# Optimization experiments

Hardware: AMD Instinct MI355X
Metric: run time of the kernel (lower is better)

## Reference

```python
import jax, jax.numpy as jnp
import numpy as np

E = 1024
B = 16
SV = 576
SL = 448


def setup_inputs() -> dict:
    key = jax.random.key(0)
    k1, k2, k3, k4, k5 = jax.random.split(key, 5)
    return {
        "vision_tokens": jax.random.normal(k1, (B, SV, E), dtype=jnp.float32),
        "language_tokens": jax.random.normal(k2, (B, SL, E), dtype=jnp.float32),
        "Wv": jax.random.normal(k3, (E, E), dtype=jnp.float32) * 0.02,  # vision_proj.weight
        "Wl": jax.random.normal(k4, (E, E), dtype=jnp.float32) * 0.02,  # language_proj.weight
        "Wo": jax.random.normal(k5, (E, E), dtype=jnp.float32) * 0.02,  # out_proj.weight
        "bo": jnp.zeros((E,), dtype=jnp.float32),                        # out_proj.bias
    }


def reference(vision_tokens, language_tokens, Wv, Wl, Wo, bo):
    # Separate modality projections (nn.Linear, no bias): y = x @ W.T
    vp = jnp.einsum("bsd,ed->bse", vision_tokens, Wv)
    lp = jnp.einsum("bsd,ed->bse", language_tokens, Wl)
    # Concat vision+language tokens along sequence dim
    x = jnp.concatenate([vp, lp], axis=1)  # [B, SV+SL, E]
    scale = x.shape[-1] ** -0.5  # 1/sqrt(embed_dim), single-head as in CPU path
    scores = jnp.einsum("bqe,bke->bqk", x, x) * scale
    attn = jax.nn.softmax(scores, axis=-1)
    attended = jnp.einsum("bqk,bke->bqe", attn, x)
    # out_proj (with bias)
    return jnp.einsum("bse,fe->bsf", attended, Wo) + bo
```

## Files before the change

### kernel.cpp

```cpp
#include <hip/hip_runtime.h>

typedef _Float16 f16;
typedef _Float16 f16x4 __attribute__((ext_vector_type(4)));
typedef _Float16 f16x8 __attribute__((ext_vector_type(8)));
typedef float f32x4 __attribute__((ext_vector_type(4)));

#define AS1(p) ((const __attribute__((address_space(1))) void*)(p))
#define AS3(p) ((__attribute__((address_space(3))) void*)(p))
#define BAR() { asm volatile("" ::: "memory"); __builtin_amdgcn_s_barrier(); \
                asm volatile("" ::: "memory"); __builtin_amdgcn_sched_barrier(0); }
#define VMCNT(n) asm volatile("s_waitcnt vmcnt(" #n ")" ::: "memory")


__global__ void conv_f32_to_f16(const float* __restrict__ src, f16* __restrict__ dst, long n4) {
  long i = (long)blockIdx.x * blockDim.x + threadIdx.x;
  if (i >= n4) return;
  const float4 v = ((const float4*)src)[i];
  f16x4 o = { (f16)v.x, (f16)v.y, (f16)v.z, (f16)v.w };
  ((f16x4*)dst)[i] = o;
}

__global__ void conv_tokens(const float* __restrict__ src, f16* __restrict__ dst,
                            int rpb, long dstOff, long n4) {
  long i = (long)blockIdx.x * blockDim.x + threadIdx.x;
  if (i >= n4) return;
  long perB = (long)rpb * 256;
  long b = i / perB, off = i % perB;
  const float4 v = ((const float4*)src)[i];
  f16x4 o = { (f16)v.x, (f16)v.y, (f16)v.z, (f16)v.w };
  ((f16x4*)(dst + b * 1024 * 1024 + dstOff))[off] = o;
}

template<int OUTF>
__global__ __launch_bounds__(512, 2)
void gemm256(const f16* __restrict__ A, const f16* __restrict__ Bw,
             void* __restrict__ Cv, const float* __restrict__ bias,
             int M, long sA, long sB, long sC, float scale)
{
  constexpr int K = 1024, N = 1024, T = K / 64;
  __shared__ __align__(16) char lds[131072];
  const int bz = blockIdx.z;
  const f16* Ab = A + (long)bz * sA;
  const f16* Bb = Bw + (long)bz * sB;
  const int t = threadIdx.x;
  const int w = t >> 6, l = t & 63;
  const int wr = w >> 2, wc = w & 3;
  const int brow = blockIdx.y * 256, bcol = blockIdx.x * 256;

  f32x4 acc[2][4][2][2] = {};

  const int srow = t >> 3;
  const int scol = ((t & 7) * 8) ^ (((t >> 5) & 1) << 4) ^ (((t >> 6) & 1) << 5);
  const int xmask = (((l >> 2) & 1) << 5) | (((l >> 3) & 1) << 6);
  const int lrow = l & 15, lslot = (l >> 4) * 16;

  auto stageA = [&](int kt, int h) {
    char* dst = lds + (kt & 1) * 65536 + h * 16384;
    #pragma unroll
    for (int j = 0; j < 2; ++j) {
      int ar = brow + h * 128 + j * 64 + srow;
      if (ar >= M) ar = M - 1;
      const f16* g = Ab + (long)ar * K + kt * 64 + scol;
      __builtin_amdgcn_global_load_lds(AS1(g), AS3(dst + j * 8192 + t * 16), 16, 0, 0);
    }
  };
  auto stageB = [&](int kt, int h) {
    char* dst = lds + (kt & 1) * 65536 + 32768 + h * 16384;
    #pragma unroll
    for (int j = 0; j < 2; ++j) {
      int br = bcol + h * 128 + j * 64 + srow;
      const f16* g = Bb + (long)br * K + kt * 64 + scol;
      __builtin_amdgcn_global_load_lds(AS1(g), AS3(dst + j * 8192 + t * 16), 16, 0, 0);
    }
  };
  auto ldA = [&](int kt, int mh, f16x8* a) {
    const char* base = lds + (kt & 1) * 65536;
    #pragma unroll
    for (int m4 = 0; m4 < 4; ++m4)
      #pragma unroll
      for (int kk = 0; kk < 2; ++kk) {
        int rowA = mh * 128 + wr * 64 + m4 * 16 + lrow;
        int off = (rowA * 128 + kk * 64 + lslot) ^ xmask;
        a[m4 * 2 + kk] = *(const f16x8*)(base + off);
      }
  };
  auto ldB = [&](int kt, int nh, f16x8* b) {
    const char* base = lds + (kt & 1) * 65536 + 32768;
    #pragma unroll
    for (int n2 = 0; n2 < 2; ++n2)
      #pragma unroll
      for (int kk = 0; kk < 2; ++kk) {
        int rowB = nh * 128 + wc * 32 + n2 * 16 + lrow;
        int off = (rowB * 128 + kk * 64 + lslot) ^ xmask;
        b[n2 * 2 + kk] = *(const f16x8*)(base + off);
      }
  };
  auto mma = [&](int mh, int nh, const f16x8* a, const f16x8* b) {
    __builtin_amdgcn_s_setprio(1);
    #pragma unroll
    for (int m4 = 0; m4 < 4; ++m4)
      #pragma unroll
      for (int n2 = 0; n2 < 2; ++n2)
        #pragma unroll
        for (int kk = 0; kk < 2; ++kk)
          acc[mh][m4][nh][n2] = __builtin_amdgcn_mfma_f32_16x16x32_f16(
              a[m4 * 2 + kk], b[n2 * 2 + kk], acc[mh][m4][nh][n2], 0, 0, 0);
    __builtin_amdgcn_s_setprio(0);
  };

  stageA(0, 0); stageA(0, 1); stageB(0, 0); stageB(0, 1);
  stageA(1, 0); stageB(1, 1);
  VMCNT(4);
  BAR();

  f16x8 a[8], b0[4], b1[4];
  for (int kt = 0; kt < T; ++kt) {
    ldA(kt, 0, a); ldB(kt, 0, b0);
    if (kt + 1 < T) stageA(kt + 1, 1);
    BAR();
    mma(0, 0, a, b0);
    BAR();
    ldB(kt, 1, b1);
    if (kt + 1 < T) stageB(kt + 1, 0);
    BAR();
    mma(0, 1, a, b1);
    BAR();
    ldA(kt, 1, a);
    if (kt + 2 < T) stageA(kt + 2, 0);
    BAR();
    mma(1, 1, a, b1);
    BAR();
    if (kt + 2 < T) {
      stageB(kt + 2, 1);
      VMCNT(4);
    } else if (kt + 1 < T) {
      VMCNT(0);
    }
    BAR();
    mma(1, 0, a, b0);
    BAR();
  }

  const int rj = (l >> 4) * 4;
  #pragma unroll
  for (int mh = 0; mh < 2; ++mh)
    #pragma unroll
    for (int m4 = 0; m4 < 4; ++m4)
      #pragma unroll
      for (int j = 0; j < 4; ++j) {
        const int r = brow + mh * 128 + wr * 64 + m4 * 16 + rj + j;
        if (r >= M) continue;
        #pragma unroll
        for (int nh = 0; nh < 2; ++nh)
          #pragma unroll
          for (int n2 = 0; n2 < 2; ++n2) {
            const int c = bcol + nh * 128 + wc * 32 + n2 * 16 + lrow;
            float v = acc[mh][m4][nh][n2][j];
            if constexpr (OUTF == 0) {
              ((f16*)Cv)[(long)bz * sC + (long)r * N + c] = (f16)v;
            } else if constexpr (OUTF == 1) {
              ((f16*)Cv)[(long)bz * sC + (long)r * N + c] = (f16)(v * scale);
            } else {
              ((float*)Cv)[(long)bz * sC + (long)r * N + c] = v + bias[c];
            }
          }
      }
}

__global__ __launch_bounds__(256)
void softmax_rows(f16* __restrict__ S) {
  const long row = blockIdx.x;
  f16* p = S + row * 1024;
  const int t = threadIdx.x;
  f16x4 v4 = ((f16x4*)p)[t];
  float v[4];
  #pragma unroll
  for (int j = 0; j < 4; ++j) v[j] = (float)v4[j];

  float m = fmaxf(fmaxf(v[0], v[1]), fmaxf(v[2], v[3]));
  #pragma unroll
  for (int off = 1; off < 64; off <<= 1) m = fmaxf(m, __shfl_xor(m, off));
  __shared__ float sm[4], ss[4];
  const int w = t >> 6;
  if ((t & 63) == 0) sm[w] = m;
  __syncthreads();
  m = fmaxf(fmaxf(sm[0], sm[1]), fmaxf(sm[2], sm[3]));

  float e[4], s = 0.f;
  #pragma unroll
  for (int j = 0; j < 4; ++j) { e[j] = __expf(v[j] - m); s += e[j]; }
  #pragma unroll
  for (int off = 1; off < 64; off <<= 1) s += __shfl_xor(s, off);
  if ((t & 63) == 0) ss[w] = s;
  __syncthreads();
  s = ss[0] + ss[1] + ss[2] + ss[3];
  const float inv = 1.f / s;

  f16x4 o;
  #pragma unroll
  for (int j = 0; j < 4; ++j) o[j] = (f16)(e[j] * inv);
  ((f16x4*)p)[t] = o;
}

__global__ void transpose_f16(const f16* __restrict__ in, f16* __restrict__ out) {
  __shared__ f16 tile[32][33];
  const long bs = (long)blockIdx.z * 1024 * 1024;
  const int r0 = blockIdx.y * 32, c0 = blockIdx.x * 32;
  const int tx = threadIdx.x, ty = threadIdx.y;
  #pragma unroll
  for (int i = 0; i < 4; ++i)
    tile[ty + 8 * i][tx] = in[bs + (long)(r0 + ty + 8 * i) * 1024 + c0 + tx];
  __syncthreads();
  #pragma unroll
  for (int i = 0; i < 4; ++i)
    out[bs + (long)(c0 + ty + 8 * i) * 1024 + r0 + tx] = tile[tx][ty + 8 * i];
}

extern "C" void kernel_launch(void* const* d_in, const int* in_sizes, int n_in,
                              void* d_out, int out_size, void* d_ws, size_t ws_size,
                              hipStream_t stream) {
  const float* vis = (const float*)d_in[0];
  const float* lan = (const float*)d_in[1];
  const float* Wv  = (const float*)d_in[2];
  const float* Wl  = (const float*)d_in[3];
  const float* Wo  = (const float*)d_in[4];
  const float* bo  = (const float*)d_in[5];
  float* out = (float*)d_out;

  const long PB = 1024l * 1024;
  const long SE = 16 * PB;

  f16* Ah  = (f16*)d_ws;
  f16* Xh  = Ah + SE;
  f16* Sc  = Xh + SE;
  f16* Wvh = Sc + SE;
  f16* Wlh = Wvh + PB;
  f16* Woh = Wlh + PB;
  f16* XhT = Ah;
  f16* Att = Xh;

  {
    long n4 = 16l * 576 * 1024 / 4;
    conv_tokens<<<dim3((n4 + 255) / 256), 256, 0, stream>>>(vis, Ah, 576, 0, n4);
  }
  {
    long n4 = 16l * 448 * 1024 / 4;
    conv_tokens<<<dim3((n4 + 255) / 256), 256, 0, stream>>>(lan, Ah, 448, 576l * 1024, n4);
  }
  {
    long n4 = PB / 4;
    conv_f32_to_f16<<<dim3((n4 + 255) / 256), 256, 0, stream>>>(Wv, Wvh, n4);
    conv_f32_to_f16<<<dim3((n4 + 255) / 256), 256, 0, stream>>>(Wl, Wlh, n4);
    conv_f32_to_f16<<<dim3((n4 + 255) / 256), 256, 0, stream>>>(Wo, Woh, n4);
  }
  gemm256<0><<<dim3(4, 3, 16), 512, 0, stream>>>(Ah, Wvh, Xh, nullptr, 576, PB, 0, PB, 1.f);
  gemm256<0><<<dim3(4, 2, 16), 512, 0, stream>>>(Ah + 576l * 1024, Wlh, Xh + 576l * 1024,
                                                 nullptr, 448, PB, 0, PB, 1.f);
  gemm256<1><<<dim3(4, 4, 16), 512, 0, stream>>>(Xh, Xh, Sc, nullptr, 1024, PB, PB, PB,
                                                 0.03125f);
  transpose_f16<<<dim3(32, 32, 16), dim3(32, 8), 0, stream>>>(Xh, XhT);
  softmax_rows<<<dim3(16 * 1024), 256, 0, stream>>>(Sc);
  gemm256<0><<<dim3(4, 4, 16), 512, 0, stream>>>(Sc, XhT, Att, nullptr, 1024, PB, PB, PB, 1.f);
  gemm256<2><<<dim3(4, 64, 1), 512, 0, stream>>>(Att, Woh, out, bo, 16384, 0, 0, 0, 1.f);
}
```

Baseline: 355.2 us.

## Remap GEMM blocks so each XCD handles whole batch chunks and change the LDS swizzle

Replaces the 3D grid with a 1D grid and a block-id mapping that groups the tiles of a batch (or a row chunk of the output projection) onto the same XCD. The aim is better L2 reuse of shared A/B panels. It also swaps the XOR swizzle for a row-based 8-way 16-byte swizzle to cut LDS bank conflicts on the fragment reads. The mapping depends on the grid sizes and parameters agreeing exactly, so any mismatch would leave tiles uncomputed.

```diff
diff --git a/kernel.cpp b/kernel.cpp
--- a/kernel.cpp
+++ b/kernel.cpp
@@ -35,23 +35,31 @@
 __global__ __launch_bounds__(512, 2)
 void gemm256(const f16* __restrict__ A, const f16* __restrict__ Bw,
              void* __restrict__ Cv, const float* __restrict__ bias,
-             int M, long sA, long sB, long sC, float scale)
+             int M, long sA, long sB, long sC, float scale,
+             int GX, int CHY, int NBYC, int CPG)
 {
   constexpr int K = 1024, N = 1024, T = K / 64;
   __shared__ __align__(16) char lds[131072];
-  const int bz = blockIdx.z;
+
+  const int id = blockIdx.x;
+  const int xcd = id & 7, q = id >> 3;
+  const int wi = q % CPG, ghi = q / CPG;
+  const int g = xcd + 8 * ghi;
+  const int bchunk = g % NBYC, bz = g / NBYC;
+  const int bx = wi % GX, by = bchunk * CHY + wi / GX;
+
   const f16* Ab = A + (long)bz * sA;
   const f16* Bb = Bw + (long)bz * sB;
   const int t = threadIdx.x;
   const int w = t >> 6, l = t & 63;
   const int wr = w >> 2, wc = w & 3;
-  const int brow = blockIdx.y * 256, bcol = blockIdx.x * 256;
+  const int brow = by * 256, bcol = bx * 256;
 
   f32x4 acc[2][4][2][2] = {};
 
   const int srow = t >> 3;
-  const int scol = ((t & 7) * 8) ^ (((t >> 5) & 1) << 4) ^ (((t >> 6) & 1) << 5);
-  const int xmask = (((l >> 2) & 1) << 5) | (((l >> 3) & 1) << 6);
+  const int scol = ((t & 7) * 8) ^ (((t >> 3) & 7) << 3);
+  const int xm = (l & 7) << 4;
   const int lrow = l & 15, lslot = (l >> 4) * 16;
 
   auto stageA = [&](int kt, int h) {
@@ -60,8 +68,8 @@
     for (int j = 0; j < 2; ++j) {
       int ar = brow + h * 128 + j * 64 + srow;
       if (ar >= M) ar = M - 1;
-      const f16* g = Ab + (long)ar * K + kt * 64 + scol;
-      __builtin_amdgcn_global_load_lds(AS1(g), AS3(dst + j * 8192 + t * 16), 16, 0, 0);
+      const f16* gp = Ab + (long)ar * K + kt * 64 + scol;
+      __builtin_amdgcn_global_load_lds(AS1(gp), AS3(dst + j * 8192 + t * 16), 16, 0, 0);
     }
   };
   auto stageB = [&](int kt, int h) {
@@ -69,8 +77,8 @@
     #pragma unroll
     for (int j = 0; j < 2; ++j) {
       int br = bcol + h * 128 + j * 64 + srow;
-      const f16* g = Bb + (long)br * K + kt * 64 + scol;
-      __builtin_amdgcn_global_load_lds(AS1(g), AS3(dst + j * 8192 + t * 16), 16, 0, 0);
+      const f16* gp = Bb + (long)br * K + kt * 64 + scol;
+      __builtin_amdgcn_global_load_lds(AS1(gp), AS3(dst + j * 8192 + t * 16), 16, 0, 0);
     }
   };
   auto ldA = [&](int kt, int mh, f16x8* a) {
@@ -80,7 +88,7 @@
       #pragma unroll
       for (int kk = 0; kk < 2; ++kk) {
         int rowA = mh * 128 + wr * 64 + m4 * 16 + lrow;
-        int off = (rowA * 128 + kk * 64 + lslot) ^ xmask;
+        int off = (rowA * 128 + kk * 64 + lslot) ^ xm;
         a[m4 * 2 + kk] = *(const f16x8*)(base + off);
       }
   };
@@ -91,7 +99,7 @@
       #pragma unroll
       for (int kk = 0; kk < 2; ++kk) {
         int rowB = nh * 128 + wc * 32 + n2 * 16 + lrow;
-        int off = (rowB * 128 + kk * 64 + lslot) ^ xmask;
+        int off = (rowB * 128 + kk * 64 + lslot) ^ xm;
         b[n2 * 2 + kk] = *(const f16x8*)(base + off);
       }
   };
@@ -253,13 +261,17 @@
     conv_f32_to_f16<<<dim3((n4 + 255) / 256), 256, 0, stream>>>(Wl, Wlh, n4);
     conv_f32_to_f16<<<dim3((n4 + 255) / 256), 256, 0, stream>>>(Wo, Woh, n4);
   }
-  gemm256<0><<<dim3(4, 3, 16), 512, 0, stream>>>(Ah, Wvh, Xh, nullptr, 576, PB, 0, PB, 1.f);
-  gemm256<0><<<dim3(4, 2, 16), 512, 0, stream>>>(Ah + 576l * 1024, Wlh, Xh + 576l * 1024,
-                                                 nullptr, 448, PB, 0, PB, 1.f);
-  gemm256<1><<<dim3(4, 4, 16), 512, 0, stream>>>(Xh, Xh, Sc, nullptr, 1024, PB, PB, PB,
-                                                 0.03125f);
+  gemm256<0><<<dim3(192), 512, 0, stream>>>(Ah, Wvh, Xh, nullptr, 576, PB, 0, PB, 1.f,
+                                            4, 1, 3, 4);
+  gemm256<0><<<dim3(128), 512, 0, stream>>>(Ah + 576l * 1024, Wlh, Xh + 576l * 1024,
+                                            nullptr, 448, PB, 0, PB, 1.f,
+                                            4, 1, 2, 4);
+  gemm256<1><<<dim3(256), 512, 0, stream>>>(Xh, Xh, Sc, nullptr, 1024, PB, PB, PB,
+                                            0.03125f, 4, 4, 1, 16);
   transpose_f16<<<dim3(32, 32, 16), dim3(32, 8), 0, stream>>>(Xh, XhT);
   softmax_rows<<<dim3(16 * 1024), 256, 0, stream>>>(Sc);
-  gemm256<0><<<dim3(4, 4, 16), 512, 0, stream>>>(Sc, XhT, Att, nullptr, 1024, PB, PB, PB, 1.f);
-  gemm256<2><<<dim3(4, 64, 1), 512, 0, stream>>>(Att, Woh, out, bo, 16384, 0, 0, 0, 1.f);
-}
+  gemm256<0><<<dim3(256), 512, 0, stream>>>(Sc, XhT, Att, nullptr, 1024, PB, PB, PB, 1.f,
+                                            4, 4, 1, 16);
+  gemm256<2><<<dim3(256), 512, 0, stream>>>(Att, Woh, out, bo, 16384, 0, 0, 0, 1.f,
+                                            4, 8, 8, 32);
+}
```

Measured after the change: 340.7 us. 4.1% less time.
